# Kernel tuning notes

Hardware: AMD Instinct MI355X
Metric: run time of the kernel (lower is better)

## Reference

```python
import jax, jax.numpy as jnp
import numpy as np

B, S, E, H = 4, 1024, 1024, 16
D = E // H  # head_dim = 64
SCALE = float(np.sqrt(D))


def setup_inputs() -> dict:
    key = jax.random.key(0)
    ks = jax.random.split(key, 12)
    lim = 1.0 / np.sqrt(E)  # torch nn.Linear default init range

    def lin(kw, kb):
        W = jax.random.uniform(kw, (E, E), jnp.float32, -lim, lim)
        b = jax.random.uniform(kb, (E,), jnp.float32, -lim, lim)
        return W, b

    W0, b0 = lin(ks[0], ks[1])
    W1, b1 = lin(ks[2], ks[3])
    W2, b2 = lin(ks[4], ks[5])
    Wv, bv = lin(ks[6], ks[7])
    Wo, bo = lin(ks[8], ks[9])
    A = jax.random.normal(ks[10], (D, D, D), jnp.float32)  # torch.randn core tensor
    x = jax.random.normal(ks[11], (B, S, E), jnp.float32)
    return {"x": x, "W0": W0, "b0": b0, "W1": W1, "b1": b1, "W2": W2, "b2": b2,
            "Wv": Wv, "bv": bv, "Wo": Wo, "bo": bo, "A": A}


def _heads(h):
    # (B,S,E) -> (B,H,S,D)
    return h.reshape(B, S, H, D).transpose(0, 2, 1, 3)


def reference(x, W0, b0, W1, b1, W2, b2, Wv, bv, Wo, bo, A):
    p0 = _heads(x @ W0.T + b0)
    p1 = _heads(x @ W1.T + b1)
    p2 = _heads(x @ W2.T + b2)
    # N=3 multilinear attention score: third projection is contracted over its
    # own sequence index k (faithful to the original einsum construction).
    logits = jnp.einsum('acd,bhia,bhjc,bhkd->bhij', A, p0, p1, p2,
                        optimize=True) / SCALE  # (B,H,S,S)
    attn = jax.nn.softmax(logits, axis=-1)  # dropout inactive (eval / p=0)
    v = _heads(x @ Wv.T + bv)
    values = jnp.einsum('bhij,bhjd->bhid', attn, v)  # (B,H,S,D)
    values = values.transpose(0, 2, 1, 3).reshape(B, S, E)
    out = values @ Wo.T + bo
    return out, attn
```

## Files before the change

kernel.cpp:

```cpp
#include <hip/hip_runtime.h>
#include <hip/hip_bf16.h>
#include <cstddef>

#define B_ 4
#define S_ 1024
#define E_ 1024
#define H_ 16
#define D_ 64
#define BH_ (B_*H_)

typedef __attribute__((ext_vector_type(8))) short short8;
typedef __attribute__((ext_vector_type(4))) float f32x4;
typedef __attribute__((ext_vector_type(4))) unsigned short us4;
typedef unsigned short u16;

__device__ inline u16 f2b(float x) {
    return __builtin_bit_cast(u16, __float2bfloat16(x));
}
__device__ inline float b2f(u16 u) {
    return __bfloat162float(__builtin_bit_cast(__hip_bfloat16, u));
}
__device__ inline void splitf(float x, u16& h, u16& l) {
    h = f2b(x); l = f2b(x - b2f(h));
}

__device__ inline void split_one(const float* __restrict__ in,
                                 u16* __restrict__ oh, u16* __restrict__ ol, int i)
{
    float4 v = ((const float4*)in)[i];
    us4 h, l;
    splitf(v.x, ((u16*)&h)[0], ((u16*)&l)[0]);
    splitf(v.y, ((u16*)&h)[1], ((u16*)&l)[1]);
    splitf(v.z, ((u16*)&h)[2], ((u16*)&l)[2]);
    splitf(v.w, ((u16*)&h)[3], ((u16*)&l)[3]);
    ((us4*)oh)[i] = h;
    ((us4*)ol)[i] = l;
}

__device__ inline void conv_one(const float* __restrict__ in,
                                u16* __restrict__ ob, int i)
{
    float4 v = ((const float4*)in)[i];
    us4 h;
    ((u16*)&h)[0] = f2b(v.x); ((u16*)&h)[1] = f2b(v.y);
    ((u16*)&h)[2] = f2b(v.z); ((u16*)&h)[3] = f2b(v.w);
    ((us4*)ob)[i] = h;
}

__global__ __launch_bounds__(256) void prep(
    const float* __restrict__ x, const float* __restrict__ W0,
    const float* __restrict__ W1, const float* __restrict__ Wv,
    const float* __restrict__ Wo, float* __restrict__ xsum_p,
    u16* __restrict__ xh, u16* __restrict__ xl,
    u16* __restrict__ w0h, u16* __restrict__ w0l,
    u16* __restrict__ w1h, u16* __restrict__ w1l,
    u16* __restrict__ wvb, u16* __restrict__ wob)
{
    int bid = blockIdx.x, tid = threadIdx.x;
    if (bid < 4096) {
        split_one(x, xh, xl, bid * 256 + tid);
    } else if (bid < 5120) {
        split_one(W0, w0h, w0l, (bid - 4096) * 256 + tid);
    } else if (bid < 6144) {
        split_one(W1, w1h, w1l, (bid - 5120) * 256 + tid);
    } else if (bid < 7168) {
        conv_one(Wv, wvb, (bid - 6144) * 256 + tid);
    } else if (bid < 8192) {
        conv_one(Wo, wob, (bid - 7168) * 256 + tid);
    } else {
        int p = bid - 8192;
        int kb = p & 3, b = (p >> 2) & 3, ch = p >> 4;
        int k = kb * 256 + tid;
        const float* base = x + ((size_t)(b * S_ + ch * 64)) * E_ + k;
        float s = 0.f;
#pragma unroll 8
        for (int j = 0; j < 64; ++j) s += base[(size_t)j * E_];
        xsum_p[(ch * 4 + b) * E_ + k] = s;
    }
}

__global__ __launch_bounds__(256) void t2k_M(
    const float* __restrict__ W2, const float* __restrict__ b2v,
    const float* __restrict__ xsum_p, const float* __restrict__ A,
    u16* __restrict__ MTh, u16* __restrict__ MTl)
{
    int h = blockIdx.x, b = blockIdx.y, tid = threadIdx.x;
    __shared__ float xs[1024];
    __shared__ float t2s[64];

#pragma unroll
    for (int j = 0; j < 4; ++j) {
        int k = j * 256 + tid;
        float s = 0.f;
#pragma unroll
        for (int c = 0; c < 16; ++c) s += xsum_p[(c * 4 + b) * E_ + k];
        xs[k] = s;
    }
    __syncthreads();

    int w = tid >> 6, lane = tid & 63;
    for (int nn = w; nn < 64; nn += 4) {
        int n = h * 64 + nn;
        const float* wr = W2 + (size_t)n * E_;
        float s = 0.f;
#pragma unroll
        for (int t = 0; t < 16; ++t) s = fmaf(wr[t * 64 + lane], xs[t * 64 + lane], s);
#pragma unroll
        for (int off = 1; off < 64; off <<= 1) s += __shfl_xor(s, off, 64);
        if (lane == 0) t2s[nn] = s + 1024.0f * b2v[n];
    }
    __syncthreads();

    int bh = b * H_ + h;
    int c = tid & 63;
    int a0 = (tid >> 6) * 16;
    for (int a = a0; a < a0 + 16; ++a) {
        float s = 0.f;
        const float* Ap = A + ((size_t)a * 64 + c) * 64;
#pragma unroll 8
        for (int d = 0; d < 64; ++d) s = fmaf(Ap[d], t2s[d], s);
        u16 hh, ll; splitf(s * 0.125f, hh, ll);
        MTh[(size_t)bh * 4096 + c * 64 + a] = hh;
        MTl[(size_t)bh * 4096 + c * 64 + a] = ll;
    }
}

__device__ void qp1_body(
    const u16* __restrict__ Xh, const u16* __restrict__ Xl,
    const u16* __restrict__ W0h_, const u16* __restrict__ W0l_,
    const u16* __restrict__ W1h_, const u16* __restrict__ W1l_,
    const float* __restrict__ bias0, const float* __restrict__ bias1,
    const u16* __restrict__ MTh, const u16* __restrict__ MTl,
    u16* __restrict__ qh, u16* __restrict__ ql,
    u16* __restrict__ p1h, u16* __restrict__ p1l,
    int bm, int bn, char* smem)
{
    const int K = 1024;
    u16* Xs_h  = (u16*)smem;
    u16* Xs_l  = Xs_h + 128 * 40;
    u16* W0s_h = Xs_l + 128 * 40;
    u16* W0s_l = W0s_h + 64 * 40;
    u16* W1s_h = W0s_l + 64 * 40;
    u16* W1s_l = W1s_h + 64 * 40;
    u16* Cs_h  = (u16*)smem;
    u16* Cs_l  = Cs_h + 128 * 72;

    const int tid = threadIdx.x;
    const int w = tid >> 6, lane = tid & 63;
    const int waveM = w & 1, waveN = w >> 1;
    const int quad = lane >> 4, l16 = lane & 15;

    const int xrow = tid >> 1, xko = (tid & 1) * 16;
    const int wrow = tid >> 2, wko = (tid & 3) * 8;

    const u16* xh_g  = Xh  + (size_t)(bm * 128 + xrow) * K + xko;
    const u16* xl_g  = Xl  + (size_t)(bm * 128 + xrow) * K + xko;
    const u16* w0h_g = W0h_ + (size_t)(bn * 64 + wrow) * K + wko;
    const u16* w0l_g = W0l_ + (size_t)(bn * 64 + wrow) * K + wko;
    const u16* w1h_g = W1h_ + (size_t)(bn * 64 + wrow) * K + wko;
    const u16* w1l_g = W1l_ + (size_t)(bn * 64 + wrow) * K + wko;

    f32x4 acc0[4][2] = {};
    f32x4 acc1[4][2] = {};

    for (int k0 = 0; k0 < K; k0 += 32) {
        uint4 xa = *(const uint4*)(xh_g + k0);
        uint4 xb = *(const uint4*)(xh_g + k0 + 8);
        uint4 xc = *(const uint4*)(xl_g + k0);
        uint4 xd = *(const uint4*)(xl_g + k0 + 8);
        uint4 w0a = *(const uint4*)(w0h_g + k0);
        uint4 w0c = *(const uint4*)(w0l_g + k0);
        uint4 w1a = *(const uint4*)(w1h_g + k0);
        uint4 w1c = *(const uint4*)(w1l_g + k0);
        __syncthreads();
        *(uint4*)&Xs_h[xrow * 40 + xko]     = xa;
        *(uint4*)&Xs_h[xrow * 40 + xko + 8] = xb;
        *(uint4*)&Xs_l[xrow * 40 + xko]     = xc;
        *(uint4*)&Xs_l[xrow * 40 + xko + 8] = xd;
        *(uint4*)&W0s_h[wrow * 40 + wko] = w0a;
        *(uint4*)&W0s_l[wrow * 40 + wko] = w0c;
        *(uint4*)&W1s_h[wrow * 40 + wko] = w1a;
        *(uint4*)&W1s_l[wrow * 40 + wko] = w1c;
        __syncthreads();

        short8 ah[4], al[4], b0h[2], b0l[2], b1h[2], b1l[2];
#pragma unroll
        for (int mt = 0; mt < 4; ++mt) {
            int r = (waveM * 64 + mt * 16 + l16) * 40 + quad * 8;
            ah[mt] = *(short8*)&Xs_h[r];
            al[mt] = *(short8*)&Xs_l[r];
        }
#pragma unroll
        for (int nt = 0; nt < 2; ++nt) {
            int r = (waveN * 32 + nt * 16 + l16) * 40 + quad * 8;
            b0h[nt] = *(short8*)&W0s_h[r];
            b0l[nt] = *(short8*)&W0s_l[r];
            b1h[nt] = *(short8*)&W1s_h[r];
            b1l[nt] = *(short8*)&W1s_l[r];
        }
#pragma unroll
        for (int mt = 0; mt < 4; ++mt)
#pragma unroll
            for (int nt = 0; nt < 2; ++nt) {
                acc0[mt][nt] = __builtin_amdgcn_mfma_f32_16x16x32_bf16(ah[mt], b0h[nt], acc0[mt][nt], 0, 0, 0);
                acc1[mt][nt] = __builtin_amdgcn_mfma_f32_16x16x32_bf16(ah[mt], b1h[nt], acc1[mt][nt], 0, 0, 0);
                acc0[mt][nt] = __builtin_amdgcn_mfma_f32_16x16x32_bf16(ah[mt], b0l[nt], acc0[mt][nt], 0, 0, 0);
                acc1[mt][nt] = __builtin_amdgcn_mfma_f32_16x16x32_bf16(ah[mt], b1l[nt], acc1[mt][nt], 0, 0, 0);
                acc0[mt][nt] = __builtin_amdgcn_mfma_f32_16x16x32_bf16(al[mt], b0h[nt], acc0[mt][nt], 0, 0, 0);
                acc1[mt][nt] = __builtin_amdgcn_mfma_f32_16x16x32_bf16(al[mt], b1h[nt], acc1[mt][nt], 0, 0, 0);
            }
    }

    const int bh = (bm >> 3) * H_ + bn;

#pragma unroll
    for (int mt = 0; mt < 4; ++mt)
#pragma unroll
        for (int nt = 0; nt < 2; ++nt)
#pragma unroll
            for (int r = 0; r < 4; ++r) {
                int m = bm * 128 + waveM * 64 + mt * 16 + quad * 4 + r;
                int n = bn * 64 + waveN * 32 + nt * 16 + l16;
                float val = acc1[mt][nt][r] + bias1[n];
                int s = m & 1023, c = n & 63;
                size_t addr = ((size_t)bh * S_ + s) * 64 + c;
                u16 hh, ll; splitf(val, hh, ll);
                p1h[addr] = hh; p1l[addr] = ll;
            }

    __syncthreads();
#pragma unroll
    for (int mt = 0; mt < 4; ++mt)
#pragma unroll
        for (int nt = 0; nt < 2; ++nt)
#pragma unroll
            for (int r = 0; r < 4; ++r) {
                int i = waveM * 64 + mt * 16 + quad * 4 + r;
                int a = waveN * 32 + nt * 16 + l16;
                float val = acc0[mt][nt][r] + bias0[bn * 64 + a];
                u16 hh, ll; splitf(val, hh, ll);
                Cs_h[i * 72 + a] = hh;
                Cs_l[i * 72 + a] = ll;
            }
    __syncthreads();

    const u16* MTh_b = MTh + (size_t)bh * 4096;
    const u16* MTl_b = MTl + (size_t)bh * 4096;
    f32x4 qacc[4][2] = {};
#pragma unroll
    for (int ch = 0; ch < 2; ++ch) {
        short8 mh[2], ml[2];
#pragma unroll
        for (int nt = 0; nt < 2; ++nt) {
            int c = waveN * 32 + nt * 16 + l16;
            mh[nt] = *(const short8*)&MTh_b[c * 64 + ch * 32 + quad * 8];
            ml[nt] = *(const short8*)&MTl_b[c * 64 + ch * 32 + quad * 8];
        }
#pragma unroll
        for (int mt = 0; mt < 4; ++mt) {
            int rr = (waveM * 64 + mt * 16 + l16) * 72 + ch * 32 + quad * 8;
            short8 ca = *(short8*)&Cs_h[rr];
            short8 cl = *(short8*)&Cs_l[rr];
#pragma unroll
            for (int nt = 0; nt < 2; ++nt) {
                qacc[mt][nt] = __builtin_amdgcn_mfma_f32_16x16x32_bf16(ca, mh[nt], qacc[mt][nt], 0, 0, 0);
                qacc[mt][nt] = __builtin_amdgcn_mfma_f32_16x16x32_bf16(ca, ml[nt], qacc[mt][nt], 0, 0, 0);
                qacc[mt][nt] = __builtin_amdgcn_mfma_f32_16x16x32_bf16(cl, mh[nt], qacc[mt][nt], 0, 0, 0);
            }
        }
    }
#pragma unroll
    for (int mt = 0; mt < 4; ++mt)
#pragma unroll
        for (int nt = 0; nt < 2; ++nt)
#pragma unroll
            for (int r = 0; r < 4; ++r) {
                int s = (bm & 7) * 128 + waveM * 64 + mt * 16 + quad * 4 + r;
                int c = waveN * 32 + nt * 16 + l16;
                size_t addr = ((size_t)bh * S_ + s) * 64 + c;
                u16 hh, ll; splitf(qacc[mt][nt][r], hh, ll);
                qh[addr] = hh; ql[addr] = ll;
            }
}

__device__ void plain128_body(
    const u16* __restrict__ Xb, const u16* __restrict__ Wb,
    const float* __restrict__ bias, u16* __restrict__ outB,
    float* __restrict__ outF, int mode, int bm, int bn, char* smem)
{
    const int K = 1024;
    u16* Xs = (u16*)smem;
    u16* Ws = Xs + 128 * 40;

    const int tid = threadIdx.x;
    const int w = tid >> 6, lane = tid & 63;
    const int waveM = w & 1, waveN = w >> 1;
    const int quad = lane >> 4, l16 = lane & 15;
    const int xrow = tid >> 1, xko = (tid & 1) * 16;
    const int wrow = tid >> 2, wko = (tid & 3) * 8;

    const u16* xg = Xb + (size_t)(bm * 128 + xrow) * K + xko;
    const u16* wg = Wb + (size_t)(bn * 64 + wrow) * K + wko;

    f32x4 acc[4][2] = {};

    for (int k0 = 0; k0 < K; k0 += 32) {
        uint4 xa = *(const uint4*)(xg + k0);
        uint4 xb = *(const uint4*)(xg + k0 + 8);
        uint4 wa = *(const uint4*)(wg + k0);
        __syncthreads();
        *(uint4*)&Xs[xrow * 40 + xko]     = xa;
        *(uint4*)&Xs[xrow * 40 + xko + 8] = xb;
        *(uint4*)&Ws[wrow * 40 + wko]     = wa;
        __syncthreads();

        short8 af[4], bf_[2];
#pragma unroll
        for (int mt = 0; mt < 4; ++mt)
            af[mt] = *(short8*)&Xs[(waveM * 64 + mt * 16 + l16) * 40 + quad * 8];
#pragma unroll
        for (int nt = 0; nt < 2; ++nt)
            bf_[nt] = *(short8*)&Ws[(waveN * 32 + nt * 16 + l16) * 40 + quad * 8];
#pragma unroll
        for (int mt = 0; mt < 4; ++mt)
#pragma unroll
            for (int nt = 0; nt < 2; ++nt)
                acc[mt][nt] = __builtin_amdgcn_mfma_f32_16x16x32_bf16(af[mt], bf_[nt], acc[mt][nt], 0, 0, 0);
    }

#pragma unroll
    for (int mt = 0; mt < 4; ++mt)
#pragma unroll
        for (int nt = 0; nt < 2; ++nt)
#pragma unroll
            for (int r = 0; r < 4; ++r) {
                int m = bm * 128 + waveM * 64 + mt * 16 + quad * 4 + r;
                int n = bn * 64 + waveN * 32 + nt * 16 + l16;
                float val = acc[mt][nt][r] + bias[n];
                if (mode == 0) {
                    int b = m >> 10, s = m & 1023, h = n >> 6, c = n & 63;
                    outB[((size_t)((b * H_ + h) * 64 + c)) * S_ + s] = f2b(val);
                } else {
                    outF[(size_t)m * 1024 + n] = val;
                }
            }
}

__global__ __launch_bounds__(256) void gemm_mid(
    const u16* __restrict__ xh, const u16* __restrict__ xl,
    const u16* __restrict__ w0h, const u16* __restrict__ w0l,
    const u16* __restrict__ w1h, const u16* __restrict__ w1l,
    const float* __restrict__ b0, const float* __restrict__ b1,
    const u16* __restrict__ MTh, const u16* __restrict__ MTl,
    u16* __restrict__ qh, u16* __restrict__ ql,
    u16* __restrict__ p1h, u16* __restrict__ p1l,
    const u16* __restrict__ wvb, const float* __restrict__ bv,
    u16* __restrict__ vT)
{
    __shared__ __align__(16) char smem[40960];
    int bid = blockIdx.x;
    if (bid < 512) {
        qp1_body(xh, xl, w0h, w0l, w1h, w1l, b0, b1, MTh, MTl,
                 qh, ql, p1h, p1l, bid & 31, bid >> 5, smem);
    } else {
        int b2 = bid - 512;
        plain128_body(xh, wvb, bv, vT, nullptr, 0, b2 & 31, b2 >> 5, smem);
    }
}

__global__ __launch_bounds__(256) void gemm_fin(
    const u16* __restrict__ values, const u16* __restrict__ wob,
    const float* __restrict__ bo, float* __restrict__ out)
{
    __shared__ __align__(16) char smem[15360];
    plain128_body(values, wob, bo, nullptr, out, 1, blockIdx.x, blockIdx.y, smem);
}

__global__ __launch_bounds__(512) void logits_softmax_pv(
    const u16* __restrict__ qh, const u16* __restrict__ ql,
    const u16* __restrict__ p1h, const u16* __restrict__ p1l,
    const u16* __restrict__ vT, float* __restrict__ attn,
    u16* __restrict__ values)
{
    int bh = blockIdx.x, i0 = blockIdx.y * 32;
    int b = bh >> 4, h = bh & 15;
    int tid = threadIdx.x, w = tid >> 6, lane = tid & 63;
    int quad = lane >> 4, l16 = lane & 15;
    int wg = w >> 2, wj = w & 3;

    __shared__ __align__(16) char sm[65536];
    float* redm = (float*)sm;
    float* reds = (float*)(sm + 512);

    short8 ah[2], al[2];
    {
        size_t gq = ((size_t)bh * S_ + i0 + wg * 16 + l16) * 64 + quad * 8;
        ah[0] = *(const short8*)&qh[gq];
        ah[1] = *(const short8*)&qh[gq + 32];
        al[0] = *(const short8*)&ql[gq];
        al[1] = *(const short8*)&ql[gq + 32];
    }

    const size_t gpb = ((size_t)bh * S_ + wj * 16 + l16) * 64 + quad * 8;
    f32x4 L[16];
#pragma unroll
    for (int t = 0; t < 16; ++t) {
        size_t g = gpb + (size_t)t * 4096;
        short8 bh0 = *(const short8*)&p1h[g];
        short8 bh1 = *(const short8*)&p1h[g + 32];
        short8 bl0 = *(const short8*)&p1l[g];
        short8 bl1 = *(const short8*)&p1l[g + 32];
        f32x4 a = {};
        a = __builtin_amdgcn_mfma_f32_16x16x32_bf16(ah[0], bh0, a, 0, 0, 0);
        a = __builtin_amdgcn_mfma_f32_16x16x32_bf16(ah[1], bh1, a, 0, 0, 0);
        a = __builtin_amdgcn_mfma_f32_16x16x32_bf16(ah[0], bl0, a, 0, 0, 0);
        a = __builtin_amdgcn_mfma_f32_16x16x32_bf16(ah[1], bl1, a, 0, 0, 0);
        a = __builtin_amdgcn_mfma_f32_16x16x32_bf16(al[0], bh0, a, 0, 0, 0);
        a = __builtin_amdgcn_mfma_f32_16x16x32_bf16(al[1], bh1, a, 0, 0, 0);
        L[t] = a;
    }

    float mrow[4], srow[4];
#pragma unroll
    for (int r = 0; r < 4; ++r) {
        float m = L[0][r];
#pragma unroll
        for (int t = 1; t < 16; ++t) m = fmaxf(m, L[t][r]);
#pragma unroll
        for (int off = 1; off < 16; off <<= 1) m = fmaxf(m, __shfl_xor(m, off, 64));
        mrow[r] = m;
    }
    if (l16 == 0)
#pragma unroll
        for (int r = 0; r < 4; ++r) redm[wj * 32 + wg * 16 + quad * 4 + r] = mrow[r];
    __syncthreads();
#pragma unroll
    for (int r = 0; r < 4; ++r) {
        int rowg = wg * 16 + quad * 4 + r;
        float m = fmaxf(fmaxf(redm[0 * 32 + rowg], redm[1 * 32 + rowg]),
                        fmaxf(redm[2 * 32 + rowg], redm[3 * 32 + rowg]));
        float s = 0.f;
#pragma unroll
        for (int t = 0; t < 16; ++t) { L[t][r] = __expf(L[t][r] - m); s += L[t][r]; }
#pragma unroll
        for (int off = 1; off < 16; off <<= 1) s += __shfl_xor(s, off, 64);
        srow[r] = s;
    }
    if (l16 == 0)
#pragma unroll
        for (int r = 0; r < 4; ++r) reds[wj * 32 + wg * 16 + quad * 4 + r] = srow[r];
    __syncthreads();
#pragma unroll
    for (int r = 0; r < 4; ++r) {
        int rowg = wg * 16 + quad * 4 + r;
        float inv = 1.0f / (reds[0 * 32 + rowg] + reds[1 * 32 + rowg] +
                            reds[2 * 32 + rowg] + reds[3 * 32 + rowg]);
        float* arow = attn + ((size_t)bh * S_ + i0 + rowg) * S_;
#pragma unroll
        for (int t = 0; t < 16; ++t) {
            float p = L[t][r] * inv;
            L[t][r] = p;
            __builtin_nontemporal_store(p, &arow[t * 64 + wj * 16 + l16]);
        }
    }

    __syncthreads();
    {
        int row = wg * 16 + quad * 4;
        int colb = (wj * 16 + l16) * 2;
#pragma unroll
        for (int t = 0; t < 16; ++t)
#pragma unroll
            for (int r = 0; r < 4; ++r) {
                int off = (t * 128 + colb) ^ (((row + r) & 7) << 4);
                *(u16*)(sm + (row + r) * 2048 + off) = f2b(L[t][r]);
            }
    }
    __syncthreads();

    const int d = wj * 16 + l16;
    const int arow = wg * 16 + l16;
    const char* Pr = sm + arow * 2048;
    const int rxor = (arow & 7) << 4;
    const size_t gvb = (size_t)(bh * 64 + d) * S_ + quad * 8;
    f32x4 acc_pv = {};
#pragma unroll
    for (int t = 0; t < 16; ++t)
#pragma unroll
        for (int cc = 0; cc < 64; cc += 32) {
            short8 af = *(const short8*)(Pr + ((t * 128 + cc * 2 + quad * 16) ^ rxor));
            short8 bf = *(const short8*)&vT[gvb + t * 64 + cc];
            acc_pv = __builtin_amdgcn_mfma_f32_16x16x32_bf16(af, bf, acc_pv, 0, 0, 0);
        }
#pragma unroll
    for (int r = 0; r < 4; ++r) {
        int i = i0 + wg * 16 + quad * 4 + r;
        values[((size_t)(b * S_ + i)) * E_ + h * 64 + d] = f2b(acc_pv[r]);
    }
}

extern "C" void kernel_launch(void* const* d_in, const int* in_sizes, int n_in,
                              void* d_out, int out_size, void* d_ws, size_t ws_size,
                              hipStream_t stream)
{
    const float* x  = (const float*)d_in[0];
    const float* W0 = (const float*)d_in[1];
    const float* b0 = (const float*)d_in[2];
    const float* W1 = (const float*)d_in[3];
    const float* b1 = (const float*)d_in[4];
    const float* W2 = (const float*)d_in[5];
    const float* b2 = (const float*)d_in[6];
    const float* Wv = (const float*)d_in[7];
    const float* bv = (const float*)d_in[8];
    const float* Wo = (const float*)d_in[9];
    const float* bo = (const float*)d_in[10];
    const float* A  = (const float*)d_in[11];

    float* out  = (float*)d_out;
    float* attn = out + (size_t)B_ * S_ * E_;

    u16* xh  = (u16*)d_ws;
    u16* xl  = xh + 4194304;
    u16* w0h = xl + 4194304;
    u16* w0l = w0h + 1048576;
    u16* w1h = w0l + 1048576;
    u16* w1l = w1h + 1048576;
    u16* p1h = w1l + 1048576;
    u16* p1l = p1h + 4194304;
    u16* qh  = p1l + 4194304;
    u16* ql  = qh + 4194304;
    u16* vT  = ql + 4194304;
    u16* values = vT + 4194304;
    u16* MTh = values + 4194304;
    u16* MTl = MTh + 262144;
    u16* wob = MTl + 262144;
    float* xsum_p = (float*)p1h;
    u16* wvb = values;

    prep<<<8448, 256, 0, stream>>>(x, W0, W1, Wv, Wo, xsum_p,
                                   xh, xl, w0h, w0l, w1h, w1l, wvb, wob);
    t2k_M<<<dim3(16, 4), 256, 0, stream>>>(W2, b2, xsum_p, A, MTh, MTl);

    gemm_mid<<<1024, 256, 0, stream>>>(xh, xl, w0h, w0l, w1h, w1l,
                                       b0, b1, MTh, MTl, qh, ql, p1h, p1l,
                                       wvb, bv, vT);

    logits_softmax_pv<<<dim3(64, 32), 512, 0, stream>>>(qh, ql, p1h, p1l, vT, attn, values);

    gemm_fin<<<dim3(32, 16), 256, 0, stream>>>(values, wob, bo, out);
}
```

Baseline: 647.4 us.

## Stage p1 tiles through double-buffered LDS with register prefetch in logits kernel

The logits loop previously had each wave load its own p1 hi/lo rows directly from global memory, so the two wave groups fetched the same rows twice. The block now loads each 64-row p1 chunk cooperatively into padded shared memory, double-buffers it, and prefetches two chunks ahead into registers. MFMA operands are then read from LDS. This trades duplicate global traffic for a barrier on every iteration. The `#pragma unroll` on this loop was also removed, which could leave the L[] accumulator array dynamically indexed and push it to scratch memory.

```diff
diff --git a/kernel.cpp b/kernel.cpp
--- a/kernel.cpp
+++ b/kernel.cpp
@@ -389,8 +389,10 @@
     int wg = w >> 2, wj = w & 3;
 
     __shared__ __align__(16) char sm[65536];
-    float* redm = (float*)sm;
-    float* reds = (float*)(sm + 512);
+    u16* p1hs = (u16*)sm;
+    u16* p1ls = (u16*)(sm + 18432);
+    float* redm = (float*)(sm + 36864);
+    float* reds = (float*)(sm + 37376);
 
     short8 ah[2], al[2];
     {
@@ -401,15 +403,33 @@
         al[1] = *(const short8*)&ql[gq + 32];
     }
 
-    const size_t gpb = ((size_t)bh * S_ + wj * 16 + l16) * 64 + quad * 8;
+    const int jl = tid >> 3, c0s = (tid & 7) * 8;
+    const size_t gp = ((size_t)bh * S_ + jl) * 64 + c0s;
+
+    uint4 rha = *(const uint4*)&p1h[gp];
+    uint4 rla = *(const uint4*)&p1l[gp];
+    *(uint4*)&p1hs[jl * 72 + c0s] = rha;
+    *(uint4*)&p1ls[jl * 72 + c0s] = rla;
+    uint4 rh1 = *(const uint4*)&p1h[gp + 4096];
+    uint4 rl1 = *(const uint4*)&p1l[gp + 4096];
+    __syncthreads();
+
     f32x4 L[16];
-#pragma unroll
     for (int t = 0; t < 16; ++t) {
-        size_t g = gpb + (size_t)t * 4096;
-        short8 bh0 = *(const short8*)&p1h[g];
-        short8 bh1 = *(const short8*)&p1h[g + 32];
-        short8 bl0 = *(const short8*)&p1l[g];
-        short8 bl1 = *(const short8*)&p1l[g + 32];
+        int cur = t & 1;
+        uint4 rh2, rl2;
+        if (t < 14) {
+            size_t gn = gp + (size_t)(t + 2) * 4096;
+            rh2 = *(const uint4*)&p1h[gn];
+            rl2 = *(const uint4*)&p1l[gn];
+        }
+        int jr = wj * 16 + l16;
+        const u16* Hb = &p1hs[cur * 4608 + jr * 72];
+        const u16* Lb = &p1ls[cur * 4608 + jr * 72];
+        short8 bh0 = *(const short8*)(Hb + quad * 8);
+        short8 bh1 = *(const short8*)(Hb + 32 + quad * 8);
+        short8 bl0 = *(const short8*)(Lb + quad * 8);
+        short8 bl1 = *(const short8*)(Lb + 32 + quad * 8);
         f32x4 a = {};
         a = __builtin_amdgcn_mfma_f32_16x16x32_bf16(ah[0], bh0, a, 0, 0, 0);
         a = __builtin_amdgcn_mfma_f32_16x16x32_bf16(ah[1], bh1, a, 0, 0, 0);
@@ -418,6 +438,12 @@
         a = __builtin_amdgcn_mfma_f32_16x16x32_bf16(al[0], bh0, a, 0, 0, 0);
         a = __builtin_amdgcn_mfma_f32_16x16x32_bf16(al[1], bh1, a, 0, 0, 0);
         L[t] = a;
+        if (t < 15) {
+            *(uint4*)&p1hs[(1 - cur) * 4608 + jl * 72 + c0s] = rh1;
+            *(uint4*)&p1ls[(1 - cur) * 4608 + jl * 72 + c0s] = rl1;
+            if (t < 14) { rh1 = rh2; rl1 = rl2; }
+            __syncthreads();
+        }
     }
 
     float mrow[4], srow[4];
```

Result: faster. 593.0 us (-8.4%).
